# Kernel tuning notes

Hardware: AMD Instinct MI355X
Metric: run time of the kernel (lower is better)

Reference implementation:

```python
import jax, jax.numpy as jnp
import numpy as np

N_R, N_C = 20000, 5000
E_R, E_C = 320000, 80000
D_IN, HID, OUT, K = 6, 128, 3, 3
NEG_SLOPE = 0.2


def gat_layer(x, edge_index, W, a_src, a_dst, b):
    """PyG GATConv (heads=1, concat=True, add_self_loops=True), eval mode."""
    n = x.shape[0]
    loop = jnp.arange(n, dtype=edge_index.dtype)
    src = jnp.concatenate([edge_index[0], loop])
    dst = jnp.concatenate([edge_index[1], loop])
    h = x @ W                                   # [n, HID]
    e_src = h @ a_src                           # [n]
    e_dst = h @ a_dst
    e = jax.nn.leaky_relu(e_src[src] + e_dst[dst], NEG_SLOPE)  # [E+n]
    m = jax.ops.segment_max(e, dst, num_segments=n)
    m = jnp.where(jnp.isfinite(m), m, 0.0)
    ex = jnp.exp(e - m[dst])
    denom = jax.ops.segment_sum(ex, dst, num_segments=n)
    alpha = ex / jnp.maximum(denom[dst], 1e-16)
    return jax.ops.segment_sum(alpha[:, None] * h[src], dst, num_segments=n) + b


def setup_inputs() -> dict:
    key = jax.random.key(0)
    ks = jax.random.split(key, 32)
    inp = {
        "x_resting": jax.random.normal(ks[0], (N_R, D_IN), jnp.float32),
        "x_collider": jax.random.normal(ks[1], (N_C, D_IN), jnp.float32),
        "edge_index_resting": jax.random.randint(ks[2], (2, E_R), 0, N_R, jnp.int32),
        "edge_index_collider": jax.random.randint(ks[3], (2, E_C), 0, N_C, jnp.int32),
        "knn_k": K,
    }
    i = 4
    for g in ("r", "c"):
        d_in = D_IN
        for l in (1, 2):
            inp[f"W_{g}{l}"] = jax.random.normal(ks[i], (d_in, HID), jnp.float32) * (1.0 / np.sqrt(d_in)); i += 1
            inp[f"as_{g}{l}"] = jax.random.normal(ks[i], (HID,), jnp.float32) * 0.1; i += 1
            inp[f"ad_{g}{l}"] = jax.random.normal(ks[i], (HID,), jnp.float32) * 0.1; i += 1
            inp[f"b_{g}{l}"] = jnp.zeros((HID,), jnp.float32); i += 1
            d_in = HID
    inp["W_dec"] = jax.random.normal(ks[i], (2 * HID, OUT), jnp.float32) * (1.0 / np.sqrt(2 * HID)); i += 1
    inp["b_dec"] = jnp.zeros((OUT,), jnp.float32)
    return inp


def reference(x_resting, x_collider, edge_index_resting, edge_index_collider, knn_k,
              W_r1, as_r1, ad_r1, b_r1, W_r2, as_r2, ad_r2, b_r2,
              W_c1, as_c1, ad_c1, b_c1, W_c2, as_c2, ad_c2, b_c2,
              W_dec, b_dec):
    # resting branch (dropout is identity in eval mode)
    h_r = jax.nn.relu(gat_layer(x_resting, edge_index_resting, W_r1, as_r1, ad_r1, b_r1))
    h_r = jax.nn.relu(gat_layer(h_r, edge_index_resting, W_r2, as_r2, ad_r2, b_r2))
    # collider branch
    h_c = jax.nn.relu(gat_layer(x_collider, edge_index_collider, W_c1, as_c1, ad_c1, b_c1))
    h_c = jax.nn.relu(gat_layer(h_c, edge_index_collider, W_c2, as_c2, ad_c2, b_c2))
    # brute-force KNN: for each collider node, k nearest resting nodes (in feature space)
    d2 = (jnp.sum(h_c * h_c, 1)[:, None] + jnp.sum(h_r * h_r, 1)[None, :]
          - 2.0 * h_c @ h_r.T)                       # [N_C, N_R]
    _, nn_idx = jax.lax.top_k(-d2, knn_k)            # [N_C, k] indices into resting
    n_r = h_r.shape[0]
    flat_idx = nn_idx.reshape(-1)
    rep_c = jnp.repeat(h_c, knn_k, axis=0)           # x_collider[col]
    pooled_sum = jax.ops.segment_sum(rep_c, flat_idx, num_segments=n_r)
    cnt = jax.ops.segment_sum(jnp.ones((flat_idx.shape[0],), h_c.dtype), flat_idx, num_segments=n_r)
    pooled = pooled_sum / jnp.maximum(cnt, 1.0)[:, None]  # scatter_mean (0 for empty)
    x_combined = jnp.concatenate([h_r, pooled], axis=-1)
    return x_combined @ W_dec + b_dec                # new positions [N_R, 3]
```

## Files before the change

kernel.cpp:

```cpp
#include <hip/hip_runtime.h>
#include <hip/hip_bf16.h>

#define HID 128
#define NEG_SLOPE 0.2f
#define CSPLIT 8
#define KNN_CB 64
#define NCAND (CSPLIT * 12)
#define SEG 64

typedef _Float16 f16x8 __attribute__((ext_vector_type(8)));
typedef float f32x4 __attribute__((ext_vector_type(4)));

__device__ __forceinline__ bool cand_lt(float d1, int i1, float d2, int i2) {
    return d1 < d2 || (d1 == d2 && i1 < i2);
}
__device__ __forceinline__ void ins3(float s, int r, float fd[3], int fi[3]) {
    if (!cand_lt(s, r, fd[2], fi[2])) return;
    if (cand_lt(s, r, fd[0], fi[0])) {
        fd[2]=fd[1];fi[2]=fi[1]; fd[1]=fd[0];fi[1]=fi[0]; fd[0]=s;fi[0]=r;
    } else if (cand_lt(s, r, fd[1], fi[1])) {
        fd[2]=fd[1];fi[2]=fi[1]; fd[1]=s;fi[1]=r;
    } else {
        fd[2]=s;fi[2]=r;
    }
}

__global__ void k_deg(const int* __restrict__ ei, int E, int n, int* __restrict__ deg) {
    int i = blockIdx.x * blockDim.x + threadIdx.x;
    if (i >= E + n) return;
    int d = (i < E) ? ei[E + i] : i - E;
    atomicAdd(&deg[d], 1);
}

__global__ void k_chunksum(const int* __restrict__ deg, int* __restrict__ bsum, int n) {
    int t = threadIdx.x;
    int i = blockIdx.x * 256 + t;
    int v = (i < n) ? deg[i] : 0;
#pragma unroll
    for (int o = 1; o < 64; o <<= 1) v += __shfl_xor(v, o);
    __shared__ int wsum[4];
    if ((t & 63) == 0) wsum[t >> 6] = v;
    __syncthreads();
    if (t == 0) bsum[blockIdx.x] = wsum[0] + wsum[1] + wsum[2] + wsum[3];
}

__global__ void k_scan_small(int* __restrict__ a, int nb) {
    __shared__ int buf[256];
    int t = threadIdx.x;
    int v = (t < nb) ? a[t] : 0;
    buf[t] = v;
    __syncthreads();
    for (int o = 1; o < 256; o <<= 1) {
        int add = (t >= o) ? buf[t - o] : 0;
        __syncthreads();
        buf[t] += add;
        __syncthreads();
    }
    if (t < nb) a[t] = buf[t] - v;
    if (t == 0) a[nb] = buf[nb - 1];
}

__global__ void k_scan_apply(const int* __restrict__ deg, const int* __restrict__ bsum,
                             int* __restrict__ off, int* __restrict__ cur, int n) {
    __shared__ int buf[256];
    int b = blockIdx.x, t = threadIdx.x;
    int i = b * 256 + t;
    int v = (i < n) ? deg[i] : 0;
    buf[t] = v;
    __syncthreads();
    for (int o = 1; o < 256; o <<= 1) {
        int add = (t >= o) ? buf[t - o] : 0;
        __syncthreads();
        buf[t] += add;
        __syncthreads();
    }
    int excl = bsum[b] + buf[t] - v;
    if (i < n) { off[i] = excl; cur[i] = excl; }
    if (b == 0 && t == 0) off[n] = bsum[gridDim.x];
}

__global__ void k_scatter(const int* __restrict__ ei, int E, int n,
                          int* __restrict__ cursor, int* __restrict__ csr) {
    int i = blockIdx.x * blockDim.x + threadIdx.x;
    if (i >= E + n) return;
    int s, d;
    if (i < E) { s = ei[i]; d = ei[E + i]; } else { s = d = i - E; }
    int pos = atomicAdd(&cursor[d], 1);
    csr[pos] = s;
}

__global__ void k_nn_hist(const int* __restrict__ nn, int m, int n_r, int* __restrict__ cnt) {
    int i = blockIdx.x * blockDim.x + threadIdx.x;
    if (i >= m) return;
    int r = nn[i];
    if ((unsigned)r < (unsigned)n_r) atomicAdd(&cnt[r], 1);
}

__global__ void k_nn_scatter(const int* __restrict__ nn, int m, int n_r,
                             int* __restrict__ cur, int* __restrict__ plist) {
    int i = blockIdx.x * blockDim.x + threadIdx.x;
    if (i >= m) return;
    int r = nn[i];
    if ((unsigned)r < (unsigned)n_r) {
        int pos = atomicAdd(&cur[r], 1);
        plist[pos] = i / 3;
    }
}

__global__ void k_build_segs(const int* __restrict__ poff, int n,
                             int* __restrict__ seg_cnt,
                             int* __restrict__ seg_node, int* __restrict__ seg_off) {
    int i = blockIdx.x * blockDim.x + threadIdx.x;
    if (i >= n) return;
    int beg = poff[i], end = poff[i + 1];
    int len = end - beg;
    if (len <= 0) return;
    int nseg = (len + SEG - 1) / SEG;
    int pos = atomicAdd(seg_cnt, nseg);
    for (int s = 0; s < nseg; ++s) {
        seg_node[pos + s] = i;
        seg_off[pos + s] = beg + s * SEG;
    }
}

__global__ __launch_bounds__(256) void k_pool_seg(
    const int* __restrict__ seg_cnt, const int* __restrict__ seg_node,
    const int* __restrict__ seg_off, const int* __restrict__ poff,
    const int* __restrict__ plist, const float* __restrict__ hc,
    float* __restrict__ pooled) {
    __shared__ float red[4][HID];
    int S = *seg_cnt;
    int t = threadIdx.x, w = t >> 6, lane = t & 63;
    for (int si = blockIdx.x; si < S; si += gridDim.x) {
        int node = seg_node[si];
        int beg = seg_off[si];
        int end = min(beg + SEG, poff[node + 1]);
        float p0 = 0.f, p1 = 0.f;
        for (int j = beg + w; j < end; j += 4) {
            int c = plist[j];
            p0 += hc[(size_t)c * HID + lane];
            p1 += hc[(size_t)c * HID + 64 + lane];
        }
        red[w][lane] = p0;
        red[w][64 + lane] = p1;
        __syncthreads();
        if (w == 0) {
            float s0 = red[0][lane] + red[1][lane] + red[2][lane] + red[3][lane];
            float s1 = red[0][64 + lane] + red[1][64 + lane]
                     + red[2][64 + lane] + red[3][64 + lane];
            atomicAdd(&pooled[(size_t)node * HID + lane], s0);
            atomicAdd(&pooled[(size_t)node * HID + 64 + lane], s1);
        }
        __syncthreads();
    }
}

__global__ __launch_bounds__(128) void k_linear(
    const float* __restrict__ x, const float* __restrict__ W,
    const float* __restrict__ a_src, const float* __restrict__ a_dst,
    float* __restrict__ h, float* __restrict__ es, float* __restrict__ ed,
    int d_in, int n) {
    int n0 = blockIdx.x * 4;
    int t = threadIdx.x;
    int w = t >> 6, lane = t & 63;
    __shared__ float xs[4][HID];
    __shared__ float p1[2], p2[2];
#pragma unroll
    for (int u = 0; u < 4; ++u) {
        int node = n0 + u;
        if (t < d_in) xs[u][t] = (node < n) ? x[(size_t)node * d_in + t] : 0.f;
    }
    __syncthreads();
    float acc[4] = {0.f, 0.f, 0.f, 0.f};
    for (int k = 0; k < d_in; ++k) {
        float wv = W[k * HID + t];
#pragma unroll
        for (int u = 0; u < 4; ++u) acc[u] += xs[u][k] * wv;
    }
    float asv = a_src[t], adv = a_dst[t];
    for (int u = 0; u < 4; ++u) {
        int node = n0 + u;
        if (node >= n) break;
        h[(size_t)node * HID + t] = acc[u];
        float v1 = acc[u] * asv, v2 = acc[u] * adv;
#pragma unroll
        for (int o = 32; o > 0; o >>= 1) { v1 += __shfl_xor(v1, o); v2 += __shfl_xor(v2, o); }
        if (lane == 0) { p1[w] = v1; p2[w] = v2; }
        __syncthreads();
        if (t == 0) { es[node] = p1[0] + p1[1]; ed[node] = p2[0] + p2[1]; }
        __syncthreads();
    }
}

__global__ __launch_bounds__(256) void k_gat_csr(
    const int* __restrict__ off, const int* __restrict__ csr,
    const float* __restrict__ es, const float* __restrict__ ed,
    const float* __restrict__ h, const float* __restrict__ b,
    float* __restrict__ agg, int n,
    _Float16* __restrict__ h16, float* __restrict__ n2) {
    int node = blockIdx.x * 4 + (threadIdx.x >> 6);
    int lane = threadIdx.x & 63;
    if (node >= n) return;
    int beg = off[node], end = off[node + 1];
    float edd = ed[node];
    float m = -INFINITY;
    for (int j = beg + lane; j < end; j += 64) {
        int s = csr[j];
        float e = es[s] + edd;
        e = e > 0.f ? e : NEG_SLOPE * e;
        m = fmaxf(m, e);
    }
#pragma unroll
    for (int o = 32; o > 0; o >>= 1) m = fmaxf(m, __shfl_xor(m, o));
    float den = 0.f, a0 = 0.f, a1 = 0.f;
    int j = beg;
    for (; j + 1 < end; j += 2) {
        int s0 = csr[j], s1 = csr[j + 1];
        float e0 = es[s0] + edd;
        float e1 = es[s1] + edd;
        e0 = e0 > 0.f ? e0 : NEG_SLOPE * e0;
        e1 = e1 > 0.f ? e1 : NEG_SLOPE * e1;
        float ex0 = expf(e0 - m);
        float ex1 = expf(e1 - m);
        float h00 = h[(size_t)s0 * HID + lane];
        float h01 = h[(size_t)s0 * HID + 64 + lane];
        float h10 = h[(size_t)s1 * HID + lane];
        float h11 = h[(size_t)s1 * HID + 64 + lane];
        den += ex0 + ex1;
        a0 += ex0 * h00 + ex1 * h10;
        a1 += ex0 * h01 + ex1 * h11;
    }
    if (j < end) {
        int s0 = csr[j];
        float e0 = es[s0] + edd;
        e0 = e0 > 0.f ? e0 : NEG_SLOPE * e0;
        float ex0 = expf(e0 - m);
        den += ex0;
        a0 += ex0 * h[(size_t)s0 * HID + lane];
        a1 += ex0 * h[(size_t)s0 * HID + 64 + lane];
    }
    float inv = 1.f / fmaxf(den, 1e-16f);
    float v0 = a0 * inv + b[lane];
    float v1 = a1 * inv + b[64 + lane];
    float r0 = v0 > 0.f ? v0 : 0.f;
    float r1 = v1 > 0.f ? v1 : 0.f;
    agg[(size_t)node * HID + lane] = r0;
    agg[(size_t)node * HID + 64 + lane] = r1;
    if (h16) {
        h16[(size_t)node * HID + lane] = (_Float16)r0;
        h16[(size_t)node * HID + 64 + lane] = (_Float16)r1;
    }
    if (n2) {
        float s2 = r0 * r0 + r1 * r1;
#pragma unroll
        for (int o = 32; o > 0; o >>= 1) s2 += __shfl_xor(s2, o);
        if (lane == 0) n2[node] = s2;
    }
}

__global__ __launch_bounds__(256) void k_knn_scan(
    const _Float16* __restrict__ hr2, const _Float16* __restrict__ hc2,
    const float* __restrict__ nr2, int n_c, int n_r, int rs_chunk,
    int* __restrict__ cand_i) {
    __shared__ _Float16 lds[2][64 * HID];
    int t = threadIdx.x, w = t >> 6, lane = t & 63;
    int li = lane & 15, q = lane >> 4;
    int c0 = blockIdx.x * KNN_CB;
    int split = blockIdx.y;
    int rbeg = split * rs_chunk;
    int rows = min(rs_chunk, n_r - rbeg);
    int rend = rbeg + rows;

    if (rows <= 0) {
        int c = c0 + w * 16 + li;
        if (c < n_c) {
            size_t base = ((size_t)(c * CSPLIT + split) * 4 + q) * 3;
            for (int k = 0; k < 3; ++k) cand_i[base + k] = 0x7fffffff;
        }
        return;
    }

    f16x8 bf[4];
    {
        int c = c0 + w * 16 + li;
        int cc = min(c, n_c - 1);
#pragma unroll
        for (int ks = 0; ks < 4; ++ks)
            bf[ks] = *(const f16x8*)(hc2 + (size_t)cc * HID + ks * 32 + q * 8);
    }

    float bd[3]; int bi[3];
#pragma unroll
    for (int k = 0; k < 3; ++k) { bd[k] = INFINITY; bi[k] = 0x7fffffff; }

    int nch = (rows + 63) >> 6;

    auto STAGE = [&](int bsel, int R) {
#pragma unroll
        for (int j = 0; j < 4; ++j) {
            int row = w * 16 + j * 4 + q;
            int gr = min(R + row, n_r - 1);
            int sslot = li ^ (row & 7);
            const _Float16* src = hr2 + (size_t)gr * HID + sslot * 8;
            _Float16* dst = &lds[bsel][(w * 16 + j * 4) * HID];
            __builtin_amdgcn_global_load_lds(
                (const __attribute__((address_space(1))) void*)src,
                (__attribute__((address_space(3))) void*)dst, 16, 0, 0);
        }
    };

    STAGE(0, rbeg);
    __syncthreads();

    for (int ch = 0; ch < nch; ++ch) {
        int cur = ch & 1;
        if (ch + 1 < nch) STAGE(cur ^ 1, rbeg + (ch + 1) * 64);
        int R = rbeg + ch * 64;
        const _Float16* buf = lds[cur];
        if (R + 64 <= rend) {
            float4 nrv[4];
#pragma unroll
            for (int tt = 0; tt < 4; ++tt)
                nrv[tt] = *(const float4*)(nr2 + R + tt * 16 + q * 4);
#pragma unroll
            for (int tt = 0; tt < 4; ++tt) {
                f32x4 a0 = {0.f, 0.f, 0.f, 0.f};
                int lr = tt * 16 + li;
                int swr = lr & 7;
#pragma unroll
                for (int ks = 0; ks < 4; ++ks) {
                    f16x8 af = *(const f16x8*)(&buf[lr * HID + (((ks * 4 + q) ^ swr) << 3)]);
                    a0 = __builtin_amdgcn_mfma_f32_16x16x32_f16(af, bf[ks], a0, 0, 0, 0);
                }
                int r_base = R + tt * 16 + q * 4;
                float sv[4] = {nrv[tt].x, nrv[tt].y, nrv[tt].z, nrv[tt].w};
#pragma unroll
                for (int i = 0; i < 4; ++i)
                    ins3(sv[i] - 2.f * a0[i], r_base + i, bd, bi);
            }
        } else {
            int rows_rem = rend - R;
#pragma unroll
            for (int tt = 0; tt < 4; ++tt) {
                int br = tt * 16;
                if (br < rows_rem) {
                    f32x4 a0 = {0.f, 0.f, 0.f, 0.f};
                    int lr = br + li;
                    int swr = lr & 7;
#pragma unroll
                    for (int ks = 0; ks < 4; ++ks) {
                        f16x8 af = *(const f16x8*)(&buf[lr * HID + (((ks * 4 + q) ^ swr) << 3)]);
                        a0 = __builtin_amdgcn_mfma_f32_16x16x32_f16(af, bf[ks], a0, 0, 0, 0);
                    }
                    int r_base = R + br + q * 4;
                    float4 nrv = *(const float4*)(nr2 + r_base);
                    float sv[4] = {nrv.x, nrv.y, nrv.z, nrv.w};
#pragma unroll
                    for (int i = 0; i < 4; ++i) {
                        int r = r_base + i;
                        if (r < rend) ins3(sv[i] - 2.f * a0[i], r, bd, bi);
                    }
                }
            }
        }
        __syncthreads();
    }

    {
        int c = c0 + w * 16 + li;
        if (c < n_c) {
            size_t base = ((size_t)(c * CSPLIT + split) * 4 + q) * 3;
#pragma unroll
            for (int k = 0; k < 3; ++k) cand_i[base + k] = bi[k];
        }
    }
}

__global__ __launch_bounds__(256, 4) void k_rerank(
    const int* __restrict__ cand_i, const float* __restrict__ hc,
    const float* __restrict__ hr, const float* __restrict__ nr2,
    int n_r, int* __restrict__ nn_idx) {
    int c = blockIdx.x;
    int t = threadIdx.x;
    __shared__ float hcs[HID];
    __shared__ int ci[NCAND];
    __shared__ float sc[NCAND];
    __shared__ int scr[NCAND];
    if (t < HID) hcs[t] = hc[(size_t)c * HID + t];
    if (t < NCAND) {
        int r = cand_i[(size_t)c * NCAND + t];
        ci[t] = ((unsigned)r < (unsigned)n_r) ? r : -1;
    }
    __syncthreads();

    int k4 = t & 31;
    int g = t >> 5;
    const float4* hr4 = (const float4*)hr;
    float4 a = ((const float4*)hcs)[k4];

    int rj[12];
    float4 v[12];
#pragma unroll
    for (int p = 0; p < 12; ++p) {
        rj[p] = ci[p * 8 + g];
        v[p] = hr4[(size_t)max(rj[p], 0) * 32 + k4];
    }
    float fd[3] = {INFINITY, INFINITY, INFINITY};
    int fi[3] = {0x7fffffff, 0x7fffffff, 0x7fffffff};
#pragma unroll
    for (int p = 0; p < 12; ++p) {
        float d = a.x * v[p].x + a.y * v[p].y + a.z * v[p].z + a.w * v[p].w;
#pragma unroll
        for (int o = 1; o < 32; o <<= 1) d += __shfl_xor(d, o);
        if (k4 == 0) {
            int j = p * 8 + g;
            sc[j] = (rj[p] >= 0) ? nr2[rj[p]] - 2.f * d : INFINITY;
            scr[j] = (rj[p] >= 0) ? rj[p] : 0x7fffffff;
        }
    }
    __syncthreads();
    if (t < 64) {
        ins3(sc[t], scr[t], fd, fi);
        if (t < 32) ins3(sc[64 + t], scr[64 + t], fd, fi);
#pragma unroll
        for (int o = 1; o < 64; o <<= 1) {
            float sd0 = __shfl_xor(fd[0], o), sd1 = __shfl_xor(fd[1], o), sd2 = __shfl_xor(fd[2], o);
            int si0 = __shfl_xor(fi[0], o), si1 = __shfl_xor(fi[1], o), si2 = __shfl_xor(fi[2], o);
            ins3(sd0, si0, fd, fi);
            ins3(sd1, si1, fd, fi);
            ins3(sd2, si2, fd, fi);
        }
        if (t == 0) {
            nn_idx[c * 3 + 0] = fi[0];
            nn_idx[c * 3 + 1] = fi[1];
            nn_idx[c * 3 + 2] = fi[2];
        }
    }
}

__global__ __launch_bounds__(256) void k_pool_decode(
    const int* __restrict__ poff, const float* __restrict__ pooled,
    const float* __restrict__ hr, const float* __restrict__ Wd,
    const float* __restrict__ bd, float* __restrict__ out, int n) {
    int node = blockIdx.x * 4 + (threadIdx.x >> 6);
    int lane = threadIdx.x & 63;
    if (node >= n) return;
    int len = poff[node + 1] - poff[node];
    float inv = 1.f / fmaxf((float)len, 1.f);
    float p0 = pooled[(size_t)node * HID + lane] * inv;
    float p1 = pooled[(size_t)node * HID + 64 + lane] * inv;
    float h0 = hr[(size_t)node * HID + lane];
    float h1 = hr[(size_t)node * HID + 64 + lane];
    float a0 = h0 * Wd[lane * 3 + 0] + h1 * Wd[(64 + lane) * 3 + 0]
             + p0 * Wd[(HID + lane) * 3 + 0] + p1 * Wd[(HID + 64 + lane) * 3 + 0];
    float a1 = h0 * Wd[lane * 3 + 1] + h1 * Wd[(64 + lane) * 3 + 1]
             + p0 * Wd[(HID + lane) * 3 + 1] + p1 * Wd[(HID + 64 + lane) * 3 + 1];
    float a2 = h0 * Wd[lane * 3 + 2] + h1 * Wd[(64 + lane) * 3 + 2]
             + p0 * Wd[(HID + lane) * 3 + 2] + p1 * Wd[(HID + 64 + lane) * 3 + 2];
#pragma unroll
    for (int o = 32; o > 0; o >>= 1) {
        a0 += __shfl_xor(a0, o);
        a1 += __shfl_xor(a1, o);
        a2 += __shfl_xor(a2, o);
    }
    if (lane == 0) {
        out[(size_t)node * 3 + 0] = a0 + bd[0];
        out[(size_t)node * 3 + 1] = a1 + bd[1];
        out[(size_t)node * 3 + 2] = a2 + bd[2];
    }
}

static inline int cdiv(long long a, int b) { return (int)((a + b - 1) / b); }

extern "C" void kernel_launch(void* const* d_in, const int* in_sizes, int n_in,
                              void* d_out, int out_size, void* d_ws, size_t ws_size,
                              hipStream_t stream) {
    const float* x_r = (const float*)d_in[0];
    const float* x_c = (const float*)d_in[1];
    const int* ei_r = (const int*)d_in[2];
    const int* ei_c = (const int*)d_in[3];
    const float* W_r1 = (const float*)d_in[5];
    const float* as_r1 = (const float*)d_in[6];
    const float* ad_r1 = (const float*)d_in[7];
    const float* b_r1 = (const float*)d_in[8];
    const float* W_r2 = (const float*)d_in[9];
    const float* as_r2 = (const float*)d_in[10];
    const float* ad_r2 = (const float*)d_in[11];
    const float* b_r2 = (const float*)d_in[12];
    const float* W_c1 = (const float*)d_in[13];
    const float* as_c1 = (const float*)d_in[14];
    const float* ad_c1 = (const float*)d_in[15];
    const float* b_c1 = (const float*)d_in[16];
    const float* W_c2 = (const float*)d_in[17];
    const float* as_c2 = (const float*)d_in[18];
    const float* ad_c2 = (const float*)d_in[19];
    const float* b_c2 = (const float*)d_in[20];
    const float* W_dec = (const float*)d_in[21];
    const float* b_dec = (const float*)d_in[22];
    float* out = (float*)d_out;

    const int N_R = in_sizes[0] / 6;
    const int N_C = in_sizes[1] / 6;
    const int E_R = in_sizes[2] / 2;
    const int E_C = in_sizes[3] / 2;

    float* ws = (float*)d_ws;
    size_t off = 0;
    auto alloc = [&](size_t nf) {
        float* p = ws + off;
        off += (nf + 3) & ~(size_t)3;
        return p;
    };
    float* r_h    = alloc((size_t)N_R * HID);
    float* r_agg  = alloc((size_t)N_R * HID);
    float* c_h    = alloc((size_t)N_C * HID);
    float* c_agg  = alloc((size_t)N_C * HID);
    float* pooled = alloc((size_t)N_R * HID);
    float* r_es = alloc(N_R);
    float* r_ed = alloc(N_R);
    float* c_es = alloc(N_C);
    float* c_ed = alloc(N_C);
    float* nr2 = alloc((size_t)N_R + 512);
    _Float16* hr2 = (_Float16*)alloc((size_t)N_R * HID / 2);
    _Float16* hc2 = (_Float16*)alloc((size_t)N_C * HID / 2);
    int* cand_i = (int*)alloc((size_t)N_C * NCAND);
    int* nn_idx = (int*)alloc((size_t)N_C * 3);
    int* r_deg = (int*)alloc(N_R);
    int* r_off = (int*)alloc((size_t)N_R + 1);
    int* r_cur = (int*)alloc(N_R);
    int* r_csr = (int*)alloc((size_t)E_R + N_R);
    int* r_bsum = (int*)alloc(256);
    int* c_deg = (int*)alloc(N_C);
    int* c_off = (int*)alloc((size_t)N_C + 1);
    int* c_cur = (int*)alloc(N_C);
    int* c_csr = (int*)alloc((size_t)E_C + N_C);
    int* c_bsum = (int*)alloc(256);
    int* p_cnt = (int*)alloc(N_R);
    int* p_off = (int*)alloc((size_t)N_R + 1);
    int* p_cur = (int*)alloc(N_R);
    int* p_list = (int*)alloc((size_t)N_C * 3);
    int* p_bsum = (int*)alloc(256);
    int* s_cnt = (int*)alloc(4);
    int* s_node = (int*)alloc((size_t)N_C * 3 + 4096);
    int* s_off = (int*)alloc((size_t)N_C * 3 + 4096);
    (void)ws_size; (void)n_in; (void)out_size;

    auto build_csr = [&](const int* ei, int E, int n, int* deg, int* offp, int* cur,
                         int* csr, int* bsum) {
        hipMemsetAsync(deg, 0, (size_t)n * sizeof(int), stream);
        k_deg<<<cdiv(E + n, 256), 256, 0, stream>>>(ei, E, n, deg);
        int nb = cdiv(n, 256);
        k_chunksum<<<nb, 256, 0, stream>>>(deg, bsum, n);
        k_scan_small<<<1, 256, 0, stream>>>(bsum, nb);
        k_scan_apply<<<nb, 256, 0, stream>>>(deg, bsum, offp, cur, n);
        k_scatter<<<cdiv(E + n, 256), 256, 0, stream>>>(ei, E, n, cur, csr);
    };
    auto gat = [&](const float* x, int d_in_dim, int n, const int* offp, const int* csr,
                   const float* W, const float* as_, const float* ad_, const float* b,
                   float* h, float* es, float* ed, float* agg,
                   _Float16* h16, float* n2) {
        k_linear<<<cdiv(n, 4), 128, 0, stream>>>(x, W, as_, ad_, h, es, ed, d_in_dim, n);
        k_gat_csr<<<cdiv(n, 4), 256, 0, stream>>>(offp, csr, es, ed, h, b, agg, n, h16, n2);
    };

    build_csr(ei_r, E_R, N_R, r_deg, r_off, r_cur, r_csr, r_bsum);
    gat(x_r, 6, N_R, r_off, r_csr, W_r1, as_r1, ad_r1, b_r1, r_h, r_es, r_ed, r_agg,
        nullptr, nullptr);
    gat(r_agg, HID, N_R, r_off, r_csr, W_r2, as_r2, ad_r2, b_r2, r_h, r_es, r_ed, r_agg,
        hr2, nr2);
    build_csr(ei_c, E_C, N_C, c_deg, c_off, c_cur, c_csr, c_bsum);
    gat(x_c, 6, N_C, c_off, c_csr, W_c1, as_c1, ad_c1, b_c1, c_h, c_es, c_ed, c_agg,
        nullptr, nullptr);
    gat(c_agg, HID, N_C, c_off, c_csr, W_c2, as_c2, ad_c2, b_c2, c_h, c_es, c_ed, c_agg,
        hc2, nullptr);

    int RS = cdiv(N_R, CSPLIT * 64) * 64;
    dim3 sgrid(cdiv(N_C, KNN_CB), CSPLIT);
    k_knn_scan<<<sgrid, 256, 0, stream>>>(hr2, hc2, nr2, N_C, N_R, RS, cand_i);

    k_rerank<<<N_C, 256, 0, stream>>>(cand_i, c_agg, r_agg, nr2, N_R, nn_idx);

    {
        int m = N_C * 3;
        hipMemsetAsync(p_cnt, 0, (size_t)N_R * sizeof(int), stream);
        k_nn_hist<<<cdiv(m, 256), 256, 0, stream>>>(nn_idx, m, N_R, p_cnt);
        int nb = cdiv(N_R, 256);
        k_chunksum<<<nb, 256, 0, stream>>>(p_cnt, p_bsum, N_R);
        k_scan_small<<<1, 256, 0, stream>>>(p_bsum, nb);
        k_scan_apply<<<nb, 256, 0, stream>>>(p_cnt, p_bsum, p_off, p_cur, N_R);
        k_nn_scatter<<<cdiv(m, 256), 256, 0, stream>>>(nn_idx, m, N_R, p_cur, p_list);
        hipMemsetAsync(s_cnt, 0, sizeof(int), stream);
        hipMemsetAsync(pooled, 0, (size_t)N_R * HID * sizeof(float), stream);
        k_build_segs<<<cdiv(N_R, 256), 256, 0, stream>>>(p_off, N_R, s_cnt, s_node, s_off);
        k_pool_seg<<<2048, 256, 0, stream>>>(s_cnt, s_node, s_off, p_off, p_list,
                                             c_agg, pooled);
    }

    k_pool_decode<<<cdiv(N_R, 4), 256, 0, stream>>>(p_off, pooled, r_agg,
                                                    W_dec, b_dec, out, N_R);
}
```

Before: 612.2 us.

## Double KNN split, fuse histogram into rerank, vectorize feature loads

Raises the KNN scan column split from 8 to 16, which gives more parallel blocks and doubles the candidates the rerank kernel evaluates (now 192 per collider node). The neighbour-count histogram is folded into the rerank kernel through atomics, which removes a separate kernel launch. k_linear now reduces all four nodes together with a single barrier instead of two barriers per node. The GAT, pooling and decode kernels load and store features as float2, which changes the per-lane feature mapping to interleaved pairs.

```diff
diff --git a/kernel.cpp b/kernel.cpp
--- a/kernel.cpp
+++ b/kernel.cpp
@@ -3,12 +3,13 @@
 
 #define HID 128
 #define NEG_SLOPE 0.2f
-#define CSPLIT 8
+#define CSPLIT 16
 #define KNN_CB 64
 #define NCAND (CSPLIT * 12)
 #define SEG 64
 
 typedef _Float16 f16x8 __attribute__((ext_vector_type(8)));
+typedef _Float16 f16x2 __attribute__((ext_vector_type(2)));
 typedef float f32x4 __attribute__((ext_vector_type(4)));
 
 __device__ __forceinline__ bool cand_lt(float d1, int i1, float d2, int i2) {
@@ -87,13 +88,6 @@
     if (i < E) { s = ei[i]; d = ei[E + i]; } else { s = d = i - E; }
     int pos = atomicAdd(&cursor[d], 1);
     csr[pos] = s;
-}
-
-__global__ void k_nn_hist(const int* __restrict__ nn, int m, int n_r, int* __restrict__ cnt) {
-    int i = blockIdx.x * blockDim.x + threadIdx.x;
-    if (i >= m) return;
-    int r = nn[i];
-    if ((unsigned)r < (unsigned)n_r) atomicAdd(&cnt[r], 1);
 }
 
 __global__ void k_nn_scatter(const int* __restrict__ nn, int m, int n_r,
@@ -128,28 +122,26 @@
     const int* __restrict__ seg_off, const int* __restrict__ poff,
     const int* __restrict__ plist, const float* __restrict__ hc,
     float* __restrict__ pooled) {
-    __shared__ float red[4][HID];
+    __shared__ float2 red[4][64];
     int S = *seg_cnt;
     int t = threadIdx.x, w = t >> 6, lane = t & 63;
     for (int si = blockIdx.x; si < S; si += gridDim.x) {
         int node = seg_node[si];
         int beg = seg_off[si];
         int end = min(beg + SEG, poff[node + 1]);
-        float p0 = 0.f, p1 = 0.f;
+        float2 p = make_float2(0.f, 0.f);
         for (int j = beg + w; j < end; j += 4) {
             int c = plist[j];
-            p0 += hc[(size_t)c * HID + lane];
-            p1 += hc[(size_t)c * HID + 64 + lane];
-        }
-        red[w][lane] = p0;
-        red[w][64 + lane] = p1;
+            float2 v = ((const float2*)(hc + (size_t)c * HID))[lane];
+            p.x += v.x;
+            p.y += v.y;
+        }
+        red[w][lane] = p;
         __syncthreads();
         if (w == 0) {
-            float s0 = red[0][lane] + red[1][lane] + red[2][lane] + red[3][lane];
-            float s1 = red[0][64 + lane] + red[1][64 + lane]
-                     + red[2][64 + lane] + red[3][64 + lane];
-            atomicAdd(&pooled[(size_t)node * HID + lane], s0);
-            atomicAdd(&pooled[(size_t)node * HID + 64 + lane], s1);
+            float2 a = red[0][lane], b2 = red[1][lane], c2 = red[2][lane], d2 = red[3][lane];
+            atomicAdd(&pooled[(size_t)node * HID + 2 * lane], a.x + b2.x + c2.x + d2.x);
+            atomicAdd(&pooled[(size_t)node * HID + 2 * lane + 1], a.y + b2.y + c2.y + d2.y);
         }
         __syncthreads();
     }
@@ -164,7 +156,7 @@
     int t = threadIdx.x;
     int w = t >> 6, lane = t & 63;
     __shared__ float xs[4][HID];
-    __shared__ float p1[2], p2[2];
+    __shared__ float p1s[2][4], p2s[2][4];
 #pragma unroll
     for (int u = 0; u < 4; ++u) {
         int node = n0 + u;
@@ -178,17 +170,30 @@
         for (int u = 0; u < 4; ++u) acc[u] += xs[u][k] * wv;
     }
     float asv = a_src[t], adv = a_dst[t];
+    float v1[4], v2[4];
+#pragma unroll
     for (int u = 0; u < 4; ++u) {
         int node = n0 + u;
-        if (node >= n) break;
-        h[(size_t)node * HID + t] = acc[u];
-        float v1 = acc[u] * asv, v2 = acc[u] * adv;
-#pragma unroll
-        for (int o = 32; o > 0; o >>= 1) { v1 += __shfl_xor(v1, o); v2 += __shfl_xor(v2, o); }
-        if (lane == 0) { p1[w] = v1; p2[w] = v2; }
-        __syncthreads();
-        if (t == 0) { es[node] = p1[0] + p1[1]; ed[node] = p2[0] + p2[1]; }
-        __syncthreads();
+        if (node < n) h[(size_t)node * HID + t] = acc[u];
+        v1[u] = acc[u] * asv;
+        v2[u] = acc[u] * adv;
+    }
+#pragma unroll
+    for (int o = 32; o > 0; o >>= 1) {
+#pragma unroll
+        for (int u = 0; u < 4; ++u) {
+            v1[u] += __shfl_xor(v1[u], o);
+            v2[u] += __shfl_xor(v2[u], o);
+        }
+    }
+    if (lane == 0) {
+#pragma unroll
+        for (int u = 0; u < 4; ++u) { p1s[w][u] = v1[u]; p2s[w][u] = v2[u]; }
+    }
+    __syncthreads();
+    if (t < 4 && n0 + t < n) {
+        es[n0 + t] = p1s[0][t] + p1s[1][t];
+        ed[n0 + t] = p2s[0][t] + p2s[1][t];
     }
 }
 
@@ -212,7 +217,8 @@
     }
 #pragma unroll
     for (int o = 32; o > 0; o >>= 1) m = fmaxf(m, __shfl_xor(m, o));
-    float den = 0.f, a0 = 0.f, a1 = 0.f;
+    float den = 0.f;
+    float a0 = 0.f, a1 = 0.f;
     int j = beg;
     for (; j + 1 < end; j += 2) {
         int s0 = csr[j], s1 = csr[j + 1];
@@ -222,33 +228,33 @@
         e1 = e1 > 0.f ? e1 : NEG_SLOPE * e1;
         float ex0 = expf(e0 - m);
         float ex1 = expf(e1 - m);
-        float h00 = h[(size_t)s0 * HID + lane];
-        float h01 = h[(size_t)s0 * HID + 64 + lane];
-        float h10 = h[(size_t)s1 * HID + lane];
-        float h11 = h[(size_t)s1 * HID + 64 + lane];
+        float2 h0 = ((const float2*)(h + (size_t)s0 * HID))[lane];
+        float2 h1 = ((const float2*)(h + (size_t)s1 * HID))[lane];
         den += ex0 + ex1;
-        a0 += ex0 * h00 + ex1 * h10;
-        a1 += ex0 * h01 + ex1 * h11;
+        a0 += ex0 * h0.x + ex1 * h1.x;
+        a1 += ex0 * h0.y + ex1 * h1.y;
     }
     if (j < end) {
         int s0 = csr[j];
         float e0 = es[s0] + edd;
         e0 = e0 > 0.f ? e0 : NEG_SLOPE * e0;
         float ex0 = expf(e0 - m);
+        float2 h0 = ((const float2*)(h + (size_t)s0 * HID))[lane];
         den += ex0;
-        a0 += ex0 * h[(size_t)s0 * HID + lane];
-        a1 += ex0 * h[(size_t)s0 * HID + 64 + lane];
+        a0 += ex0 * h0.x;
+        a1 += ex0 * h0.y;
     }
     float inv = 1.f / fmaxf(den, 1e-16f);
-    float v0 = a0 * inv + b[lane];
-    float v1 = a1 * inv + b[64 + lane];
-    float r0 = v0 > 0.f ? v0 : 0.f;
-    float r1 = v1 > 0.f ? v1 : 0.f;
-    agg[(size_t)node * HID + lane] = r0;
-    agg[(size_t)node * HID + 64 + lane] = r1;
+    float2 bv = ((const float2*)b)[lane];
+    float r0 = a0 * inv + bv.x;
+    float r1 = a1 * inv + bv.y;
+    r0 = r0 > 0.f ? r0 : 0.f;
+    r1 = r1 > 0.f ? r1 : 0.f;
+    float2 rv = make_float2(r0, r1);
+    ((float2*)(agg + (size_t)node * HID))[lane] = rv;
     if (h16) {
-        h16[(size_t)node * HID + lane] = (_Float16)r0;
-        h16[(size_t)node * HID + 64 + lane] = (_Float16)r1;
+        f16x2 hv = {(_Float16)r0, (_Float16)r1};
+        ((f16x2*)(h16 + (size_t)node * HID))[lane] = hv;
     }
     if (n2) {
         float s2 = r0 * r0 + r1 * r1;
@@ -379,7 +385,7 @@
 __global__ __launch_bounds__(256, 4) void k_rerank(
     const int* __restrict__ cand_i, const float* __restrict__ hc,
     const float* __restrict__ hr, const float* __restrict__ nr2,
-    int n_r, int* __restrict__ nn_idx) {
+    int n_r, int* __restrict__ nn_idx, int* __restrict__ p_cnt) {
     int c = blockIdx.x;
     int t = threadIdx.x;
     __shared__ float hcs[HID];
@@ -398,30 +404,34 @@
     const float4* hr4 = (const float4*)hr;
     float4 a = ((const float4*)hcs)[k4];
 
-    int rj[12];
-    float4 v[12];
-#pragma unroll
-    for (int p = 0; p < 12; ++p) {
-        rj[p] = ci[p * 8 + g];
-        v[p] = hr4[(size_t)max(rj[p], 0) * 32 + k4];
-    }
-    float fd[3] = {INFINITY, INFINITY, INFINITY};
-    int fi[3] = {0x7fffffff, 0x7fffffff, 0x7fffffff};
-#pragma unroll
-    for (int p = 0; p < 12; ++p) {
-        float d = a.x * v[p].x + a.y * v[p].y + a.z * v[p].z + a.w * v[p].w;
-#pragma unroll
-        for (int o = 1; o < 32; o <<= 1) d += __shfl_xor(d, o);
-        if (k4 == 0) {
-            int j = p * 8 + g;
-            sc[j] = (rj[p] >= 0) ? nr2[rj[p]] - 2.f * d : INFINITY;
-            scr[j] = (rj[p] >= 0) ? rj[p] : 0x7fffffff;
+#pragma unroll
+    for (int bp = 0; bp < 2; ++bp) {
+        int rj[12];
+        float4 v[12];
+#pragma unroll
+        for (int p = 0; p < 12; ++p) {
+            rj[p] = ci[(bp * 12 + p) * 8 + g];
+            v[p] = hr4[(size_t)max(rj[p], 0) * 32 + k4];
+        }
+#pragma unroll
+        for (int p = 0; p < 12; ++p) {
+            float d = a.x * v[p].x + a.y * v[p].y + a.z * v[p].z + a.w * v[p].w;
+#pragma unroll
+            for (int o = 1; o < 32; o <<= 1) d += __shfl_xor(d, o);
+            if (k4 == 0) {
+                int j = (bp * 12 + p) * 8 + g;
+                sc[j] = (rj[p] >= 0) ? nr2[rj[p]] - 2.f * d : INFINITY;
+                scr[j] = (rj[p] >= 0) ? rj[p] : 0x7fffffff;
+            }
         }
     }
     __syncthreads();
     if (t < 64) {
+        float fd[3] = {INFINITY, INFINITY, INFINITY};
+        int fi[3] = {0x7fffffff, 0x7fffffff, 0x7fffffff};
         ins3(sc[t], scr[t], fd, fi);
-        if (t < 32) ins3(sc[64 + t], scr[64 + t], fd, fi);
+        ins3(sc[64 + t], scr[64 + t], fd, fi);
+        ins3(sc[128 + t], scr[128 + t], fd, fi);
 #pragma unroll
         for (int o = 1; o < 64; o <<= 1) {
             float sd0 = __shfl_xor(fd[0], o), sd1 = __shfl_xor(fd[1], o), sd2 = __shfl_xor(fd[2], o);
@@ -434,6 +444,9 @@
             nn_idx[c * 3 + 0] = fi[0];
             nn_idx[c * 3 + 1] = fi[1];
             nn_idx[c * 3 + 2] = fi[2];
+#pragma unroll
+            for (int k = 0; k < 3; ++k)
+                if (fi[k] >= 0 && fi[k] < n_r) atomicAdd(&p_cnt[fi[k]], 1);
         }
     }
 }
@@ -447,16 +460,17 @@
     if (node >= n) return;
     int len = poff[node + 1] - poff[node];
     float inv = 1.f / fmaxf((float)len, 1.f);
-    float p0 = pooled[(size_t)node * HID + lane] * inv;
-    float p1 = pooled[(size_t)node * HID + 64 + lane] * inv;
-    float h0 = hr[(size_t)node * HID + lane];
-    float h1 = hr[(size_t)node * HID + 64 + lane];
-    float a0 = h0 * Wd[lane * 3 + 0] + h1 * Wd[(64 + lane) * 3 + 0]
-             + p0 * Wd[(HID + lane) * 3 + 0] + p1 * Wd[(HID + 64 + lane) * 3 + 0];
-    float a1 = h0 * Wd[lane * 3 + 1] + h1 * Wd[(64 + lane) * 3 + 1]
-             + p0 * Wd[(HID + lane) * 3 + 1] + p1 * Wd[(HID + 64 + lane) * 3 + 1];
-    float a2 = h0 * Wd[lane * 3 + 2] + h1 * Wd[(64 + lane) * 3 + 2]
-             + p0 * Wd[(HID + lane) * 3 + 2] + p1 * Wd[(HID + 64 + lane) * 3 + 2];
+    float2 p = ((const float2*)(pooled + (size_t)node * HID))[lane];
+    p.x *= inv;
+    p.y *= inv;
+    float2 h = ((const float2*)(hr + (size_t)node * HID))[lane];
+    int d0 = 2 * lane, d1 = 2 * lane + 1;
+    float a0 = h.x * Wd[d0 * 3 + 0] + h.y * Wd[d1 * 3 + 0]
+             + p.x * Wd[(HID + d0) * 3 + 0] + p.y * Wd[(HID + d1) * 3 + 0];
+    float a1 = h.x * Wd[d0 * 3 + 1] + h.y * Wd[d1 * 3 + 1]
+             + p.x * Wd[(HID + d0) * 3 + 1] + p.y * Wd[(HID + d1) * 3 + 1];
+    float a2 = h.x * Wd[d0 * 3 + 2] + h.y * Wd[d1 * 3 + 2]
+             + p.x * Wd[(HID + d0) * 3 + 2] + p.y * Wd[(HID + d1) * 3 + 2];
 #pragma unroll
     for (int o = 32; o > 0; o >>= 1) {
         a0 += __shfl_xor(a0, o);
@@ -574,16 +588,16 @@
     gat(c_agg, HID, N_C, c_off, c_csr, W_c2, as_c2, ad_c2, b_c2, c_h, c_es, c_ed, c_agg,
         hc2, nullptr);
 
+    hipMemsetAsync(p_cnt, 0, (size_t)N_R * sizeof(int), stream);
+
     int RS = cdiv(N_R, CSPLIT * 64) * 64;
     dim3 sgrid(cdiv(N_C, KNN_CB), CSPLIT);
     k_knn_scan<<<sgrid, 256, 0, stream>>>(hr2, hc2, nr2, N_C, N_R, RS, cand_i);
 
-    k_rerank<<<N_C, 256, 0, stream>>>(cand_i, c_agg, r_agg, nr2, N_R, nn_idx);
+    k_rerank<<<N_C, 256, 0, stream>>>(cand_i, c_agg, r_agg, nr2, N_R, nn_idx, p_cnt);
 
     {
         int m = N_C * 3;
-        hipMemsetAsync(p_cnt, 0, (size_t)N_R * sizeof(int), stream);
-        k_nn_hist<<<cdiv(m, 256), 256, 0, stream>>>(nn_idx, m, N_R, p_cnt);
         int nb = cdiv(N_R, 256);
         k_chunksum<<<nb, 256, 0, stream>>>(p_cnt, p_bsum, N_R);
         k_scan_small<<<1, 256, 0, stream>>>(p_bsum, nb);
```

Result: no change. 617.9 us (+0.9%).
